# Optimization experiments

Hardware: AMD Instinct MI355X
Metric: run time of the kernel (lower is better)

## Reference

```python
import jax, jax.numpy as jnp
import numpy as np

B = 4; IN_CH = 256; HEAD_CH = 64; NUM_CLS = 3; H = 128; W = 128
NH = 4; KEY = 16; VAL = 16; OUT_CH = 2
VX = 0.1 * 8; VY = 0.1 * 8  # voxel_size[:2] * out_size_factor
DW = 1.6; DL = 3.9; STRIDE = 1
C_CTR = (HEAD_CH + 2 + NUM_CLS) * 9      # 621
C_COR = (HEAD_CH + 2 + NUM_CLS * 4) * 8  # 624
C_FG = (HEAD_CH + 2 + NUM_CLS) * 9       # 621


def _sampler_points():
    offs = np.arange(-STRIDE, STRIDE + 1, STRIDE, dtype=np.float32)
    oy, ox = np.meshgrid(offs, offs, indexing='ij')
    ctr = np.stack([ox, oy], 0).reshape(2, 9)  # pixel offsets
    cx = np.array([-DW/2, -DW/2, DW/2, DW/2, DL/2, -DL/2, DL/2, -DL/2], np.float32) / VX
    cy = np.array([DL/2, -DL/2, DL/2, -DL/2, -DW/2, -DW/2, DW/2, DW/2], np.float32) / VY
    # faithful to torch: stack(dim=1) -> [8,2] then .view(2,8) (row-major reinterpret)
    cor = np.stack([cx, cy], 1).reshape(2, 8)
    r = max(DW, DL)
    fx = np.array([-r/3, -r/3, -r/3, 0, 0, 0, r/3, r/3, r/3], np.float32) / VX
    fy = np.array([-r/3, 0, r/3, -r/3, 0, r/3, -r/3, 0, r/3], np.float32) / VY
    fg = np.stack([fx, fy], 1).reshape(2, 9)
    return jnp.asarray(ctr), jnp.asarray(cor), jnp.asarray(fg)


def _raw_grid():
    gx = jnp.arange(W, dtype=jnp.float32) + 0.5
    gy = jnp.arange(H, dtype=jnp.float32) + 0.5
    return jnp.stack([jnp.broadcast_to(gx[None, :], (H, W)),
                      jnp.broadcast_to(gy[:, None], (H, W))], 0)  # [2,H,W]


def _conv3x3(x, w, b):
    y = jax.lax.conv_general_dilated(x, w, (1, 1), 'SAME',
                                     dimension_numbers=('NCHW', 'OIHW', 'NCHW'))
    return y + b[None, :, None, None]


def _cbr3(x, w, b, s, t):  # conv3x3 + inference-mode BN (folded scale/shift) + relu
    return jax.nn.relu(_conv3x3(x, w, b) * s[None, :, None, None] + t[None, :, None, None])


def _cbr1(x, w, b, s, t):  # per-head 1x1 conv + BN + relu, w: [NH,O,C], x: [B,C,H,W]
    y = jnp.einsum('noc,bchw->nbohw', w, x) + b[:, None, :, None, None]
    return jax.nn.relu(y * s[:, None, :, None, None] + t[:, None, :, None, None])


def _sample(feats, grids):
    # feats [B,C,H,W]; grids [2,n,H,W] pixel coords. Matches F.grid_sample
    # (bilinear, zeros padding, align_corners=False): sample at pixel coord g-0.5.
    n = grids.shape[1]
    geo = jnp.stack([grids[0] / W, grids[1] / H], 0)  # recover_coords, [2,n,H,W]
    gx, gy = grids[0] - 0.5, grids[1] - 0.5
    x0f = jnp.floor(gx); y0f = jnp.floor(gy)
    dx, dy = gx - x0f, gy - y0f
    x0 = x0f.astype(jnp.int32); y0 = y0f.astype(jnp.int32)
    flat = feats.reshape(B, -1, H * W)

    def gather(xc, yc, wgt):
        valid = ((xc >= 0) & (xc < W) & (yc >= 0) & (yc < H)).astype(feats.dtype) * wgt
        idx = jnp.clip(yc, 0, H - 1) * W + jnp.clip(xc, 0, W - 1)
        v = jnp.take(flat, idx.reshape(-1), axis=2).reshape(B, -1, n, H, W)
        return v * valid[None, None]

    s = (gather(x0, y0, (1 - dx) * (1 - dy)) + gather(x0 + 1, y0, dx * (1 - dy))
         + gather(x0, y0 + 1, (1 - dx) * dy) + gather(x0 + 1, y0 + 1, dx * dy))
    geo_b = jnp.broadcast_to(geo[None], (B,) + geo.shape)
    out = jnp.concatenate([s, geo_b], axis=1)  # [B,C+2,n,H,W]
    return out.reshape(B, -1, H, W)           # channel index = c*n + p, as torch .view


def _forward(base_feats, cc_w, cc_b, cc_s, cc_t, ch_w, ch_b,
             oc_w, oc_b, oc_s, oc_t, oh_w, oh_b,
             fc_w, fc_b, fc_s, fc_t, fh_w, fh_b,
             q_w, q_b, q_s, q_t,
             ck_w, ck_b, ck_s, ck_t, cv_w, cv_b, cv_s, cv_t,
             kk_w, kk_b, kk_s, kk_t, kv_w, kv_b, kv_s, kv_t,
             fk_w, fk_b, fk_s, fk_t, fv_w, fv_b, fv_s, fv_t,
             p1_w, p1_b, p1_s, p1_t, p2_w, p2_b):
    center_feat = _cbr3(base_feats, cc_w, cc_b, cc_s, cc_t)
    center_map = _conv3x3(center_feat, ch_w, ch_b)
    corner_feat = _cbr3(base_feats, oc_w, oc_b, oc_s, oc_t)
    corner_map = _conv3x3(corner_feat, oh_w, oh_b)
    fg_feat = _cbr3(base_feats, fc_w, fc_b, fc_s, fc_t)
    fg_map = _conv3x3(fg_feat, fh_w, fh_b)

    ctr_pts, cor_pts, fg_pts = _sampler_points()
    raw = _raw_grid()
    g_ctr = raw[:, None] + ctr_pts[:, :, None, None]  # [2,9,H,W]
    g_cor = raw[:, None] + cor_pts[:, :, None, None]  # [2,8,H,W]
    g_fg = raw[:, None] + fg_pts[:, :, None, None]    # [2,9,H,W]

    cs = _sample(jnp.concatenate([center_feat, center_map], 1), g_ctr)  # [B,621,H,W]
    os_ = _sample(jnp.concatenate([corner_feat, corner_map], 1), g_cor)  # [B,624,H,W]
    fs = _sample(jnp.concatenate([fg_feat, fg_map], 1), g_fg)            # [B,621,H,W]

    q = _cbr1(base_feats, q_w, q_b, q_s, q_t)  # [NH,B,KEY,H,W]
    ck = _cbr1(cs, ck_w, ck_b, ck_s, ck_t); cv = _cbr1(cs, cv_w, cv_b, cv_s, cv_t)
    ok = _cbr1(os_, kk_w, kk_b, kk_s, kk_t); ov = _cbr1(os_, kv_w, kv_b, kv_s, kv_t)
    fk = _cbr1(fs, fk_w, fk_b, fk_s, fk_t); fv = _cbr1(fs, fv_w, fv_b, fv_s, fv_t)

    logits = jnp.stack([(q * ck).sum(2), (q * ok).sum(2), (q * fk).sum(2)], axis=2)  # [NH,B,3,H,W]
    attw = jax.nn.softmax(logits, axis=2)
    vals = jnp.stack([cv, ov, fv], axis=2)          # [NH,B,3,VAL,H,W]
    att = (attw[:, :, :, None] * vals).sum(2)       # [NH,B,VAL,H,W]

    # predict: 1x1 conv over cat([base_feats, att]) + BN + relu, then 1x1 to out_ch
    h1 = (jnp.einsum('noc,bchw->nbohw', p1_w[:, :, :IN_CH], base_feats)
          + jnp.einsum('nov,nbvhw->nbohw', p1_w[:, :, IN_CH:], att)
          + p1_b[:, None, :, None, None])
    h1 = jax.nn.relu(h1 * p1_s[:, None, :, None, None] + p1_t[:, None, :, None, None])
    pred = jnp.einsum('npo,nbohw->nbphw', p2_w, h1) + p2_b[:, None, :, None, None]
    heads = jnp.moveaxis(pred, 0, 1).reshape(B, NH * OUT_CH, H, W)
    return jnp.concatenate([center_map, corner_map, fg_map, heads], axis=1)  # [B,26,H,W]


def setup_inputs() -> dict:
    ks = iter(jax.random.split(jax.random.key(0), 80))

    def rn(shape, s=0.05):
        return jax.random.normal(next(ks), shape, jnp.float32) * s

    d = {"base_feats": jax.random.normal(next(ks), (B, IN_CH, H, W), jnp.float32)}
    for conv, head, hc in (("cc", "ch", NUM_CLS), ("oc", "oh", NUM_CLS * 4), ("fc", "fh", NUM_CLS)):
        d[conv + "_w"] = rn((HEAD_CH, IN_CH, 3, 3)); d[conv + "_b"] = rn((HEAD_CH,))
        d[conv + "_s"] = 1.0 + rn((HEAD_CH,)); d[conv + "_t"] = rn((HEAD_CH,))
        d[head + "_w"] = rn((hc, HEAD_CH, 3, 3)); d[head + "_b"] = jnp.full((hc,), -2.19, jnp.float32)
    d["q_w"] = rn((NH, KEY, IN_CH)); d["q_b"] = rn((NH, KEY))
    d["q_s"] = 1.0 + rn((NH, KEY)); d["q_t"] = rn((NH, KEY))
    for name, cin, cout in (("ck", C_CTR, KEY), ("cv", C_CTR, VAL), ("kk", C_COR, KEY),
                            ("kv", C_COR, VAL), ("fk", C_FG, KEY), ("fv", C_FG, VAL)):
        d[name + "_w"] = rn((NH, cout, cin)); d[name + "_b"] = rn((NH, cout))
        d[name + "_s"] = 1.0 + rn((NH, cout)); d[name + "_t"] = rn((NH, cout))
    d["p1_w"] = rn((NH, HEAD_CH, IN_CH + VAL)); d["p1_b"] = rn((NH, HEAD_CH))
    d["p1_s"] = 1.0 + rn((NH, HEAD_CH)); d["p1_t"] = rn((NH, HEAD_CH))
    d["p2_w"] = rn((NH, OUT_CH, HEAD_CH)); d["p2_b"] = jnp.full((NH, OUT_CH), -2.19, jnp.float32)
    return d


def reference(base_feats, cc_w, cc_b, cc_s, cc_t, ch_w, ch_b,
              oc_w, oc_b, oc_s, oc_t, oh_w, oh_b,
              fc_w, fc_b, fc_s, fc_t, fh_w, fh_b,
              q_w, q_b, q_s, q_t,
              ck_w, ck_b, ck_s, ck_t, cv_w, cv_b, cv_s, cv_t,
              kk_w, kk_b, kk_s, kk_t, kv_w, kv_b, kv_s, kv_t,
              fk_w, fk_b, fk_s, fk_t, fv_w, fv_b, fv_s, fv_t,
              p1_w, p1_b, p1_s, p1_t, p2_w, p2_b):
    return _forward(base_feats, cc_w, cc_b, cc_s, cc_t, ch_w, ch_b,
                    oc_w, oc_b, oc_s, oc_t, oh_w, oh_b,
                    fc_w, fc_b, fc_s, fc_t, fh_w, fh_b,
                    q_w, q_b, q_s, q_t,
                    ck_w, ck_b, ck_s, ck_t, cv_w, cv_b, cv_s, cv_t,
                    kk_w, kk_b, kk_s, kk_t, kv_w, kv_b, kv_s, kv_t,
                    fk_w, fk_b, fk_s, fk_t, fv_w, fv_b, fv_s, fv_t,
                    p1_w, p1_b, p1_s, p1_t, p2_w, p2_b)
```

## Files before the change

### kernel.cpp

```cpp
#include <hip/hip_runtime.h>
#include <hip/hip_bf16.h>
#include <math.h>


#define HW 16384
#define WIMG 128

typedef unsigned short ushortT;
typedef __attribute__((ext_vector_type(8))) short short8;
typedef __attribute__((ext_vector_type(4))) float floatx4;

constexpr size_t OFF_KV    = 16777216;
constexpr size_t OFF_A16   = 29360128;
constexpr size_t OFF_B16   = 38012928;
constexpr size_t OFF_CWT   = 46057216;
constexpr size_t OFF_CB    = OFF_CWT + 442368;
constexpr size_t OFF_HWT   = OFF_CB + 192;
constexpr size_t OFF_QWT   = OFF_HWT + 20736;
constexpr size_t OFF_QB    = OFF_QWT + 16384;
constexpr size_t OFF_KVW   = OFF_QB + 64;
constexpr size_t OFF_GEO   = OFF_KVW + 241664;
constexpr size_t OFF_P1WT  = OFF_GEO + 1152;
constexpr size_t OFF_P1B   = OFF_P1WT + 81920;

struct P53 { const float* p[53]; };

__device__ inline ushortT f2bf(float f) {
    unsigned u = __float_as_uint(f);
    unsigned r = (u + 0x7FFFu + ((u >> 16) & 1u)) >> 16;
    return (ushortT)r;
}
__device__ inline unsigned packbf(float a, float b) {
    return (unsigned)f2bf(a) | ((unsigned)f2bf(b) << 16);
}
__device__ inline float bf2f(ushortT u) {
    return __uint_as_float((unsigned)u << 16);
}

__device__ const float c_ox[3][9] = {
    {-1.f, 0.f, 1.f, -1.f, 0.f, 1.f, -1.f, 0.f, 1.f},
    {-1.f, 2.4375f, -1.f, -2.4375f, 1.f, 2.4375f, 1.f, -2.4375f, 0.f},
    {-1.625f, -1.625f, -1.625f, 0.f, -1.625f, 1.625f, 0.f, -1.625f, 0.f}};
__device__ const float c_oy[3][9] = {
    {-1.f, -1.f, -1.f, 0.f, 0.f, 0.f, 1.f, 1.f, 1.f},
    {2.4375f, -1.f, -2.4375f, -1.f, 2.4375f, 1.f, -2.4375f, 1.f, 0.f},
    {0.f, 0.f, 1.625f, 1.625f, -1.625f, 1.625f, 0.f, 1.625f, 1.625f}};

__device__ const int tapX_cor[16] = {-1,-1, 2, 3,-1,-1,-3,-2, 1, 1, 2, 3, 1, 1,-3,-2};
__device__ const int tapY_cor[16] = { 2, 3,-1,-1,-3,-2,-1,-1, 2, 3, 1, 1,-3,-2, 1, 1};
__device__ const int tapR_cor[16] = { 4, 5, 2, 2, 0, 1, 2, 2, 4, 5, 3, 3, 0, 1, 3, 3};

__device__ inline float cornw(float off, int X) {
    float f = floorf(off);
    float d = off - f;
    int fi = (int)f;
    return (X == fi) ? (1.f - d) : (X == fi + 1) ? d : 0.f;
}

__global__ __launch_bounds__(256) void prep_kernel(P53 ptrs, float* __restrict__ ws) {
    int i = blockIdx.x * 256 + threadIdx.x;
    const float* const* p = ptrs.p;
    if (i < 442368) {
        int tap = i / 49152, r = i % 49152;
        int g = r / 1536, r2 = r % 1536;
        int M = r2 >> 3, j = r2 & 7;
        int br = M >> 6, oc = M & 63, ic = g * 8 + j;
        float v = p[1 + 6 * br][(oc * 256 + ic) * 9 + tap] * p[3 + 6 * br][oc];
        ((ushortT*)(ws + OFF_CWT))[i] = f2bf(v);
        return;
    }
    i -= 442368;
    if (i < 192) {
        int br = i >> 6, oc = i & 63;
        ws[OFF_CB + i] = p[2 + 6 * br][oc] * p[3 + 6 * br][oc] + p[4 + 6 * br][oc];
        return;
    }
    i -= 192;
    if (i < 27648) {
        int j = i & 7, m = (i >> 3) & 15, u = (i >> 7) % 72, br = i / 9216;
        int cnt = (br == 1) ? 12 : 3;
        int t = u >> 3, g = u & 7, ic = g * 8 + j;
        const float* hw = (br == 0) ? p[5] : (br == 1) ? p[11] : p[17];
        float v = (m < cnt) ? hw[(m * 64 + ic) * 9 + t] : 0.f;
        ((ushortT*)(ws + OFF_HWT))[i] = f2bf(v);
        return;
    }
    i -= 27648;
    if (i < 16384) {
        int j = i & 7, m = (i >> 3) & 63, sg = i >> 9;
        int k = (sg >> 2) * 32 + (sg & 3) * 8 + j;
        ((ushortT*)(ws + OFF_QWT))[i] = f2bf(p[19][m * 256 + k] * p[21][m]);
        return;
    }
    i -= 16384;
    if (i < 64) { ws[OFF_QB + i] = p[20][i] * p[21][i] + p[22][i]; return; }
    i -= 64;
    if (i < 483328) {
        int j = i & 7, m = (i >> 3) & 127, ug = i >> 10;
        int br, NG, NT, n, C, chb, ul;
        if (ug < 84)       { br = 0; NG = 9; NT = 9;  n = 9; C = 67; chb = 0;  ul = ug; }
        else if (ug < 164) { br = 1; NG = 5; NT = 16; n = 8; C = 76; chb = 0;  ul = ug - 84; }
        else if (ug < 244) { br = 1; NG = 5; NT = 16; n = 8; C = 76; chb = 40; ul = ug - 164; }
        else               { br = 2; NG = 9; NT = 25; n = 9; C = 67; chb = 0;  ul = ug - 244; }
        int t = ul / NG, g = ul % NG;
        int c = chb + g * 8 + j;
        float v = 0.f;
        if (t < NT && c < C) {
            int X, Y;
            if (br == 0)      { X = t % 3 - 1; Y = t / 3 - 1; }
            else if (br == 1) { X = tapX_cor[t]; Y = tapY_cor[t]; }
            else              { X = t % 5 - 2; Y = t / 5 - 2; }
            const float* wsrc = (m < 64) ? p[23 + 8 * br] : p[27 + 8 * br];
            int mo = (m < 64) ? m : m - 64;
            float sc = (m < 64) ? p[25 + 8 * br][mo] : p[29 + 8 * br][mo];
            int Cn = (C + 2) * n;
            float s = 0.f;
            for (int pp = 0; pp < n; ++pp) {
                float ww = cornw(c_ox[br][pp], X) * cornw(c_oy[br][pp], Y);
                if (ww != 0.f) s += ww * wsrc[mo * Cn + c * n + pp];
            }
            v = s * sc;
        }
        ((ushortT*)(ws + OFF_KVW))[i] = f2bf(v);
        return;
    }
    i -= 483328;
    if (i < 1152) {
        int br = i / 384, rem = i % 384, which = rem >> 7, m = rem & 127;
        int n = (br == 1) ? 8 : 9, C = (br == 1) ? 76 : 67, Cn = (C + 2) * n;
        const float* wsrc = (m < 64) ? p[23 + 8 * br] : p[27 + 8 * br];
        int mo = (m < 64) ? m : m - 64;
        float sc = (m < 64) ? p[25 + 8 * br][mo] : p[29 + 8 * br][mo];
        float bb = (m < 64) ? p[24 + 8 * br][mo] : p[28 + 8 * br][mo];
        float tt = (m < 64) ? p[26 + 8 * br][mo] : p[30 + 8 * br][mo];
        float v = 0.f;
        if (which == 0) {
            for (int pp = 0; pp < n; ++pp) v += wsrc[mo * Cn + C * n + pp];
            v *= sc;
        } else if (which == 1) {
            for (int pp = 0; pp < n; ++pp) v += wsrc[mo * Cn + (C + 1) * n + pp];
            v *= sc;
        } else {
            for (int pp = 0; pp < n; ++pp)
                v += wsrc[mo * Cn + C * n + pp] * c_ox[br][pp]
                   + wsrc[mo * Cn + (C + 1) * n + pp] * c_oy[br][pp];
            v = v * sc * 0.0078125f + bb * sc + tt;
        }
        ws[OFF_GEO + br * 384 + which * 128 + m] = v;
        return;
    }
    i -= 1152;
    if (i < 81920) {
        int j = i & 7, M = (i >> 3) & 255, sg = i >> 11;
        int k = (sg >> 2) * 32 + (sg & 3) * 8 + j;
        int nh = M >> 6, oc = M & 63;
        float sc = p[49][nh * 64 + oc];
        float v;
        if (k < 256) v = p[47][(nh * 64 + oc) * 272 + k] * sc;
        else {
            int k2 = k - 256, nh2 = k2 >> 4, va = k2 & 15;
            v = (nh2 == nh) ? p[47][(nh * 64 + oc) * 272 + 256 + va] * sc : 0.f;
        }
        ((ushortT*)(ws + OFF_P1WT))[i] = f2bf(v);
        return;
    }
    i -= 81920;
    if (i < 256) { ws[OFF_P1B + i] = p[48][i] * p[49][i] + p[50][i]; return; }
}

__global__ __launch_bounds__(256) void pass_a(const float* __restrict__ base,
                                              ushortT* __restrict__ dst) {
    int idx = blockIdx.x * 256 + threadIdx.x;
    if (idx >= 4 * 32 * 130 * 130) return;
    int col = idx % 130, t = idx / 130;
    int row = t % 130; t /= 130;
    int icg = t & 31, b = t >> 5;
    int h = row - 1, w = col - 1;
    unsigned wds[4] = {0u, 0u, 0u, 0u};
    if ((unsigned)h < 128u && (unsigned)w < 128u) {
        const float* s = base + (size_t)(b * 256 + icg * 8) * HW + h * WIMG + w;
        #pragma unroll
        for (int jp = 0; jp < 4; ++jp)
            wds[jp] = packbf(s[(size_t)(2 * jp) * HW], s[(size_t)(2 * jp + 1) * HW]);
    }
    unsigned* d = (unsigned*)(dst + (size_t)idx * 8);
    d[0] = wds[0]; d[1] = wds[1]; d[2] = wds[2]; d[3] = wds[3];
}

__global__ __launch_bounds__(256) void border_zero(ushortT* __restrict__ b16) {
    int idx = blockIdx.x * 256 + threadIdx.x;
    if (idx >= 4 * 28 * 134 * 134) return;
    int col = idx % 134, row = (idx / 134) % 134;
    if (row < 3 || row >= 131 || col < 3 || col >= 131) {
        unsigned* d = (unsigned*)(b16 + (size_t)idx * 8);
        d[0] = 0u; d[1] = 0u; d[2] = 0u; d[3] = 0u;
    }
}

__global__ __launch_bounds__(256) void conv_base_mfma(
    const ushortT* __restrict__ a16, const ushortT* __restrict__ wA,
    const float* __restrict__ cb, ushortT* __restrict__ b16)
{
    const int wv = threadIdx.x >> 6, lane = threadIdx.x & 63;
    const int sub = lane >> 4, ln = lane & 15;
    const int xh = blockIdx.x, h = blockIdx.y, b = blockIdx.z;
    const int x0 = xh * 64;
    __shared__ __align__(16) ushortT sbuf[8 * 3 * 66 * 8];

    floatx4 acc[3][4];
    #pragma unroll
    for (int mt = 0; mt < 3; ++mt)
        #pragma unroll
        for (int nt = 0; nt < 4; ++nt)
            #pragma unroll
            for (int r = 0; r < 4; ++r) acc[mt][nt][r] = 0.f;

    for (int s = 0; s < 4; ++s) {
        __syncthreads();
        for (int it = 0; it < 7; ++it) {
            int idx = threadIdx.x + it * 256;
            if (idx < 1584) {
                int col = idx % 66, t2 = idx / 66;
                int r = t2 % 3, icg = t2 / 3;
                *(short8*)(sbuf + (size_t)idx * 8) = *(const short8*)(a16 +
                    (((size_t)(b * 32 + s * 8 + icg) * 130 + (h + r)) * 130 + (x0 + col)) * 8);
            }
        }
        __syncthreads();
        #pragma unroll
        for (int tap = 0; tap < 9; ++tap) {
            const int ky = tap / 3, kx = tap % 3;
            #pragma unroll
            for (int icc = 0; icc < 2; ++icc) {
                const int icgl = icc * 4 + sub;
                short8 Bf[4];
                #pragma unroll
                for (int nt = 0; nt < 4; ++nt) {
                    int c = nt * 16 + ln + kx;
                    Bf[nt] = *(const short8*)(sbuf + ((icgl * 3 + ky) * 66 + c) * 8);
                }
                const int g = s * 8 + icc * 4 + sub;
                short8 Af[3];
                #pragma unroll
                for (int mt = 0; mt < 3; ++mt) {
                    int m = wv * 48 + mt * 16 + ln;
                    Af[mt] = *(const short8*)(wA + (((size_t)tap * 32 + g) * 192 + m) * 8);
                }
                #pragma unroll
                for (int mt = 0; mt < 3; ++mt)
                    #pragma unroll
                    for (int nt = 0; nt < 4; ++nt)
                        acc[mt][nt] = __builtin_amdgcn_mfma_f32_16x16x32_bf16(
                            Af[mt], Bf[nt], acc[mt][nt], 0, 0, 0);
            }
        }
    }
    #pragma unroll
    for (int mt = 0; mt < 3; ++mt)
        #pragma unroll
        for (int nt = 0; nt < 4; ++nt) {
            int px = x0 + nt * 16 + ln;
            int ocq = wv * 48 + mt * 16 + sub * 4;
            float v0 = fmaxf(acc[mt][nt][0] + cb[ocq + 0], 0.f);
            float v1 = fmaxf(acc[mt][nt][1] + cb[ocq + 1], 0.f);
            float v2 = fmaxf(acc[mt][nt][2] + cb[ocq + 2], 0.f);
            float v3 = fmaxf(acc[mt][nt][3] + cb[ocq + 3], 0.f);
            int br = ocq >> 6, oc = ocq & 63;
            int grp = ((br == 0) ? 0 : (br == 1) ? 9 : 19) + (oc >> 3);
            int j0 = oc & 7;
            unsigned* d = (unsigned*)(b16 +
                (((size_t)(b * 28 + grp) * 134 + (h + 3)) * 134 + (px + 3)) * 8 + j0);
            d[0] = packbf(v0, v1); d[1] = packbf(v2, v3);
        }
}

__global__ __launch_bounds__(256) void conv_head_mfma(
    const ushortT* __restrict__ b16c, const ushortT* __restrict__ wH,
    const float* __restrict__ chb, const float* __restrict__ ohb,
    const float* __restrict__ fhb, float* __restrict__ out,
    ushortT* __restrict__ b16)
{
    const int wv = threadIdx.x >> 6, lane = threadIdx.x & 63;
    const int sub = lane >> 4, ln = lane & 15;
    const int h = blockIdx.x;
    const int br = blockIdx.y % 3, b = blockIdx.y / 3;
    const int cnt = (br == 1) ? 12 : 3;
    const int mapb = (br == 0) ? 0 : (br == 1) ? 3 : 15;
    const int grpb = (br == 0) ? 0 : (br == 1) ? 9 : 19;
    const float* bias = (br == 0) ? chb : (br == 1) ? ohb : fhb;
    __shared__ __align__(16) ushortT sbuf[8 * 3 * 130 * 8];

    for (int it = 0; it < 13; ++it) {
        int idx = threadIdx.x + it * 256;
        if (idx < 3120) {
            int col = idx % 130, t2 = idx / 130;
            int r = t2 % 3, g = t2 / 3;
            *(short8*)(sbuf + (size_t)idx * 8) = *(const short8*)(b16c +
                (((size_t)(b * 28 + grpb + g) * 134 + (h + r + 2)) * 134 + (col + 2)) * 8);
        }
    }
    __syncthreads();

    floatx4 acc[2];
    #pragma unroll
    for (int nt = 0; nt < 2; ++nt)
        #pragma unroll
        for (int r = 0; r < 4; ++r) acc[nt][r] = 0.f;
    #pragma unroll
    for (int k = 0; k < 18; ++k) {
        int u = k * 4 + sub;
        int t = u >> 3, g = u & 7;
        int dxv = t % 3 - 1, ry = t / 3;
        short8 Af = *(const short8*)(wH + ((size_t)(br * 72 + u) * 16 + ln) * 8);
        #pragma unroll
        for (int nt = 0; nt < 2; ++nt) {
            int c = wv * 32 + nt * 16 + ln + dxv + 1;
            short8 Bf = *(const short8*)(sbuf + ((g * 3 + ry) * 130 + c) * 8);
            acc[nt] = __builtin_amdgcn_mfma_f32_16x16x32_bf16(Af, Bf, acc[nt], 0, 0, 0);
        }
    }
    #pragma unroll
    for (int nt = 0; nt < 2; ++nt) {
        int px = wv * 32 + nt * 16 + ln;
        #pragma unroll
        for (int r = 0; r < 4; ++r) {
            int m = sub * 4 + r;
            if (m < cnt) {
                float v = acc[nt][r] + bias[m];
                out[((size_t)b * 26 + mapb + m) * HW + h * WIMG + px] = v;
                int grp = grpb + 8 + (m >> 3), j = m & 7;
                b16[(((size_t)(b * 28 + grp) * 134 + (h + 3)) * 134 + (px + 3)) * 8 + j]
                    = f2bf(v);
            }
        }
    }
}

template<int BR, int NGRP, int NTAP, int ROWS, int COLS, int XMIN, int NCHUNK,
         int NPH, int UBASE>
__global__ __launch_bounds__(256) void kv_conv(
    const ushortT* __restrict__ b16, const ushortT* __restrict__ wU0,
    const float* __restrict__ geo, ushortT* __restrict__ kvout)
{
    const int wv = threadIdx.x >> 6, lane = threadIdx.x & 63;
    const int sub = lane >> 4, ln = lane & 15;
    const int x0 = blockIdx.x * 64, h = blockIdx.y, b = blockIdx.z;
    __shared__ __align__(16) ushortT sbuf[NGRP * ROWS * COLS * 8];

    floatx4 acc[2][4];
    #pragma unroll
    for (int mt = 0; mt < 2; ++mt)
        #pragma unroll
        for (int nt = 0; nt < 4; ++nt)
            #pragma unroll
            for (int r = 0; r < 4; ++r) acc[mt][nt][r] = 0.f;

    #pragma unroll
    for (int ph = 0; ph < NPH; ++ph) {
        const ushortT* wU = wU0 + (size_t)ph * (NCHUNK * 4 * 1024);
        __syncthreads();
        constexpr int NELEM = NGRP * ROWS * COLS;
        for (int it = 0; it < (NELEM + 255) / 256; ++it) {
            int idx = threadIdx.x + it * 256;
            if (idx < NELEM) {
                int col = idx % COLS, t2 = idx / COLS;
                int r = t2 % ROWS, grp = t2 / ROWS;
                int dy = (ROWS == 6) ? ((r < 3) ? r - 3 : r - 2) : (r - ROWS / 2);
                const ushortT* g = b16 +
                    (((size_t)(b * 28 + UBASE + ph * NGRP + grp) * 134 + (h + dy + 3)) * 134
                     + (x0 + col + XMIN + 3)) * 8;
                *(short8*)(sbuf + (size_t)idx * 8) = *(const short8*)g;
            }
        }
        __syncthreads();
        #pragma unroll
        for (int k = 0; k < NCHUNK; ++k) {
            int u = k * 4 + sub;
            int t = u / NGRP, g = u - t * NGRP;
            if (t >= NTAP) t = 0;
            int dxv, ry;
            if (BR == 0)      { dxv = t % 3 - 1; ry = t / 3; }
            else if (BR == 1) { dxv = tapX_cor[t]; ry = tapR_cor[t]; }
            else              { dxv = t % 5 - 2; ry = t / 5; }
            int bbase = (g * ROWS + ry) * COLS + (dxv - XMIN);
            short8 Bf[4];
            #pragma unroll
            for (int nt = 0; nt < 4; ++nt)
                Bf[nt] = *(const short8*)(sbuf + (bbase + nt * 16 + ln) * 8);
            short8 Af[2];
            #pragma unroll
            for (int mt = 0; mt < 2; ++mt)
                Af[mt] = *(const short8*)(wU + ((size_t)u * 128 + wv * 32 + mt * 16 + ln) * 8);
            #pragma unroll
            for (int mt = 0; mt < 2; ++mt)
                #pragma unroll
                for (int nt = 0; nt < 4; ++nt)
                    acc[mt][nt] = __builtin_amdgcn_mfma_f32_16x16x32_bf16(
                        Af[mt], Bf[nt], acc[mt][nt], 0, 0, 0);
        }
    }
    const float fy = (h + 0.5f) * 0.0078125f;
    #pragma unroll
    for (int mt = 0; mt < 2; ++mt)
        #pragma unroll
        for (int nt = 0; nt < 4; ++nt) {
            int px = x0 + nt * 16 + ln;
            float fx = (px + 0.5f) * 0.0078125f;
            #pragma unroll
            for (int r = 0; r < 4; ++r) {
                int Mi = wv * 32 + mt * 16 + sub * 4 + r;
                float v = acc[mt][nt][r] + geo[Mi] * fx + geo[128 + Mi] * fy + geo[256 + Mi];
                kvout[((size_t)(BR * 4 + b) * 128 + Mi) * HW + h * WIMG + px] =
                    f2bf(fmaxf(v, 0.f));
            }
        }
}

__global__ __launch_bounds__(256) void attn_pred_mfma(
    float* __restrict__ ws, const float* __restrict__ p2w,
    const float* __restrict__ p2b, float* __restrict__ out)
{
    const int wv = threadIdx.x >> 6, lane = threadIdx.x & 63;
    const int sub = lane >> 4, ln = lane & 15;
    const int px0 = blockIdx.x * 64, b = blockIdx.y;
    const ushortT* wP1 = (const ushortT*)(ws + OFF_P1WT);
    const ushortT* wQ  = (const ushortT*)(ws + OFF_QWT);
    const ushortT* a16 = (const ushortT*)(ws + OFF_A16);
    const ushortT* kv = (const ushortT*)(ws + OFF_KV);
    const float* p1b = ws + OFF_P1B;
    const float* qb  = ws + OFF_QB;
    __shared__ __align__(16) ushortT xbuf[40 * 64 * 8];
    __shared__ __align__(16) ushortT qld[64 * 64];

    const int mypx = threadIdx.x & 63, nh = threadIdx.x >> 6;
    const int gpx = px0 + mypx, hh = gpx >> 7, ww = gpx & 127;
    #pragma unroll
    for (int g2 = 0; g2 < 8; ++g2) {
        int g = nh * 8 + g2;
        short8 v = *(const short8*)(a16 +
            (((size_t)(b * 32 + g) * 130 + (hh + 1)) * 130 + (ww + 1)) * 8);
        *(short8*)(xbuf + ((size_t)g * 64 + mypx) * 8) = v;
    }
    __syncthreads();

    {
        floatx4 qacc[4];
        #pragma unroll
        for (int nt = 0; nt < 4; ++nt)
            #pragma unroll
            for (int r = 0; r < 4; ++r) qacc[nt][r] = 0.f;
        #pragma unroll
        for (int kk = 0; kk < 8; ++kk) {
            short8 Af = *(const short8*)(wQ + (((kk * 4 + sub) * 64) + wv * 16 + ln) * 8);
            #pragma unroll
            for (int nt = 0; nt < 4; ++nt) {
                short8 Bf = *(const short8*)(xbuf + (((kk * 4 + sub) * 64) + nt * 16 + ln) * 8);
                qacc[nt] = __builtin_amdgcn_mfma_f32_16x16x32_bf16(Af, Bf, qacc[nt], 0, 0, 0);
            }
        }
        #pragma unroll
        for (int nt = 0; nt < 4; ++nt)
            #pragma unroll
            for (int r = 0; r < 4; ++r) {
                int row = wv * 16 + sub * 4 + r;
                qld[row * 64 + nt * 16 + ln] = f2bf(fmaxf(qacc[nt][r] + qb[row], 0.f));
            }
    }
    __syncthreads();

    {
        float l[3];
        #pragma unroll
        for (int br = 0; br < 3; ++br) {
            float s = 0.f;
            #pragma unroll
            for (int ko = 0; ko < 16; ++ko)
                s = fmaf(bf2f(qld[(nh * 16 + ko) * 64 + mypx]),
                         bf2f(kv[(size_t)((br * 4 + b) * 128 + nh * 16 + ko) * HW + gpx]), s);
            l[br] = s;
        }
        float m = fmaxf(l[0], fmaxf(l[1], l[2]));
        float e0 = __expf(l[0] - m), e1 = __expf(l[1] - m), e2 = __expf(l[2] - m);
        float inv = 1.f / (e0 + e1 + e2);
        float aw0 = e0 * inv, aw1 = e1 * inv, aw2 = e2 * inv;
        #pragma unroll
        for (int vap = 0; vap < 8; ++vap) {
            int va0 = vap * 2, va1 = vap * 2 + 1;
            float a0 =
                aw0 * bf2f(kv[(size_t)((0 * 4 + b) * 128 + 64 + nh * 16 + va0) * HW + gpx]) +
                aw1 * bf2f(kv[(size_t)((1 * 4 + b) * 128 + 64 + nh * 16 + va0) * HW + gpx]) +
                aw2 * bf2f(kv[(size_t)((2 * 4 + b) * 128 + 64 + nh * 16 + va0) * HW + gpx]);
            float a1 =
                aw0 * bf2f(kv[(size_t)((0 * 4 + b) * 128 + 64 + nh * 16 + va1) * HW + gpx]) +
                aw1 * bf2f(kv[(size_t)((1 * 4 + b) * 128 + 64 + nh * 16 + va1) * HW + gpx]) +
                aw2 * bf2f(kv[(size_t)((2 * 4 + b) * 128 + 64 + nh * 16 + va1) * HW + gpx]);
            int g = 32 + nh * 2 + (vap >> 2), wo = vap & 3;
            ((unsigned*)xbuf)[(g * 64 + mypx) * 4 + wo] = packbf(a0, a1);
        }
    }
    __syncthreads();

    floatx4 acc[4][4];
    #pragma unroll
    for (int mt = 0; mt < 4; ++mt)
        #pragma unroll
        for (int nt = 0; nt < 4; ++nt)
            #pragma unroll
            for (int r = 0; r < 4; ++r) acc[mt][nt][r] = 0.f;
    #pragma unroll
    for (int kk = 0; kk < 10; ++kk) {
        short8 Bf[4];
        #pragma unroll
        for (int nt = 0; nt < 4; ++nt)
            Bf[nt] = *(const short8*)(xbuf + (((kk * 4 + sub) * 64) + nt * 16 + ln) * 8);
        #pragma unroll
        for (int mt = 0; mt < 4; ++mt) {
            short8 Af = *(const short8*)(wP1 +
                (((size_t)(kk * 4 + sub) * 256) + wv * 64 + mt * 16 + ln) * 8);
            #pragma unroll
            for (int nt = 0; nt < 4; ++nt)
                acc[mt][nt] = __builtin_amdgcn_mfma_f32_16x16x32_bf16(Af, Bf[nt], acc[mt][nt], 0, 0, 0);
        }
    }

    float po0[4] = {0.f, 0.f, 0.f, 0.f}, po1[4] = {0.f, 0.f, 0.f, 0.f};
    #pragma unroll
    for (int mt = 0; mt < 4; ++mt)
        #pragma unroll
        for (int r = 0; r < 4; ++r) {
            int oc = mt * 16 + sub * 4 + r;
            float bias = p1b[wv * 64 + oc];
            float w0 = p2w[(wv * 2 + 0) * 64 + oc];
            float w1 = p2w[(wv * 2 + 1) * 64 + oc];
            #pragma unroll
            for (int nt = 0; nt < 4; ++nt) {
                float hv = fmaxf(acc[mt][nt][r] + bias, 0.f);
                po0[nt] = fmaf(w0, hv, po0[nt]);
                po1[nt] = fmaf(w1, hv, po1[nt]);
            }
        }
    #pragma unroll
    for (int nt = 0; nt < 4; ++nt) {
        po0[nt] += __shfl_xor(po0[nt], 16);
        po0[nt] += __shfl_xor(po0[nt], 32);
        po1[nt] += __shfl_xor(po1[nt], 16);
        po1[nt] += __shfl_xor(po1[nt], 32);
    }
    if (sub == 0) {
        #pragma unroll
        for (int nt = 0; nt < 4; ++nt) {
            int px = px0 + nt * 16 + ln;
            out[((size_t)b * 26 + 18 + wv * 2 + 0) * HW + px] = po0[nt] + p2b[wv * 2 + 0];
            out[((size_t)b * 26 + 18 + wv * 2 + 1) * HW + px] = po1[nt] + p2b[wv * 2 + 1];
        }
    }
}

extern "C" void kernel_launch(void* const* d_in, const int* in_sizes, int n_in,
                              void* d_out, int out_size, void* d_ws, size_t ws_size,
                              hipStream_t stream) {
    (void)in_sizes; (void)n_in; (void)out_size; (void)ws_size;
    float* ws  = (float*)d_ws;
    float* out = (float*)d_out;
    const float* base = (const float*)d_in[0];
    P53 ptrs;
    for (int i = 0; i < 53; ++i) ptrs.p[i] = (const float*)d_in[i];

    ushortT* a16 = (ushortT*)(ws + OFF_A16);
    ushortT* b16 = (ushortT*)(ws + OFF_B16);
    ushortT* kvb = (ushortT*)(ws + OFF_KV);

    prep_kernel<<<4115, 256, 0, stream>>>(ptrs, ws);
    pass_a<<<8450, 256, 0, stream>>>(base, a16);
    border_zero<<<7856, 256, 0, stream>>>(b16);
    conv_base_mfma<<<dim3(2, 128, 4), 256, 0, stream>>>(
        a16, (const ushortT*)(ws + OFF_CWT), ws + OFF_CB, b16);
    conv_head_mfma<<<dim3(128, 12), 256, 0, stream>>>(
        b16, (const ushortT*)(ws + OFF_HWT),
        (const float*)d_in[6], (const float*)d_in[12], (const float*)d_in[18],
        out, b16);

    const ushortT* kvw = (const ushortT*)(ws + OFF_KVW);
    kv_conv<0, 9, 9, 3, 66, -1, 21, 1, 0><<<dim3(2, 128, 4), 256, 0, stream>>>(
        b16, kvw, ws + OFF_GEO, kvb);
    kv_conv<1, 5, 16, 6, 70, -3, 20, 2, 9><<<dim3(2, 128, 4), 256, 0, stream>>>(
        b16, kvw + 86016, ws + OFF_GEO + 384, kvb);
    kv_conv<2, 9, 25, 5, 68, -2, 57, 1, 19><<<dim3(2, 128, 4), 256, 0, stream>>>(
        b16, kvw + 249856, ws + OFF_GEO + 768, kvb);

    attn_pred_mfma<<<dim3(256, 4), 256, 0, stream>>>(ws, (const float*)d_in[51],
                                                     (const float*)d_in[52], out);
}
```

Baseline: 468.6 us.

## Merge KV conv branches into one launch with register double-buffering and prefetch

The three templated kv_conv launches become a single kv_all kernel that picks the branch from blockIdx.z at runtime. Tap offsets move into a shared-memory lookup table, and the warp tiling changes to 2x2 (64 channels by 32 pixels per wave). Fragment loads are double-buffered in registers so they overlap the MFMAs. Separately, pass_a and border_zero are fused into one launch, and conv_base gets a register prefetch of the next input-channel stage. The cost is that runtime branch parameters replace compile-time constants, which may add index math and register pressure.

Result: faster. 446.7 us (-4.7%).

```diff
diff --git a/kernel.cpp b/kernel.cpp
--- a/kernel.cpp
+++ b/kernel.cpp
@@ -168,32 +168,33 @@
     if (i < 256) { ws[OFF_P1B + i] = p[48][i] * p[49][i] + p[50][i]; return; }
 }
 
-__global__ __launch_bounds__(256) void pass_a(const float* __restrict__ base,
-                                              ushortT* __restrict__ dst) {
+__global__ __launch_bounds__(256) void pass_ab(const float* __restrict__ base,
+                                               ushortT* __restrict__ a16,
+                                               ushortT* __restrict__ b16) {
     int idx = blockIdx.x * 256 + threadIdx.x;
-    if (idx >= 4 * 32 * 130 * 130) return;
-    int col = idx % 130, t = idx / 130;
-    int row = t % 130; t /= 130;
-    int icg = t & 31, b = t >> 5;
-    int h = row - 1, w = col - 1;
-    unsigned wds[4] = {0u, 0u, 0u, 0u};
-    if ((unsigned)h < 128u && (unsigned)w < 128u) {
-        const float* s = base + (size_t)(b * 256 + icg * 8) * HW + h * WIMG + w;
-        #pragma unroll
-        for (int jp = 0; jp < 4; ++jp)
-            wds[jp] = packbf(s[(size_t)(2 * jp) * HW], s[(size_t)(2 * jp + 1) * HW]);
-    }
-    unsigned* d = (unsigned*)(dst + (size_t)idx * 8);
-    d[0] = wds[0]; d[1] = wds[1]; d[2] = wds[2]; d[3] = wds[3];
-}
-
-__global__ __launch_bounds__(256) void border_zero(ushortT* __restrict__ b16) {
-    int idx = blockIdx.x * 256 + threadIdx.x;
-    if (idx >= 4 * 28 * 134 * 134) return;
-    int col = idx % 134, row = (idx / 134) % 134;
-    if (row < 3 || row >= 131 || col < 3 || col >= 131) {
-        unsigned* d = (unsigned*)(b16 + (size_t)idx * 8);
-        d[0] = 0u; d[1] = 0u; d[2] = 0u; d[3] = 0u;
+    if (idx < 4 * 32 * 130 * 130) {
+        int col = idx % 130, t = idx / 130;
+        int row = t % 130; t /= 130;
+        int icg = t & 31, b = t >> 5;
+        int h = row - 1, w = col - 1;
+        unsigned wds[4] = {0u, 0u, 0u, 0u};
+        if ((unsigned)h < 128u && (unsigned)w < 128u) {
+            const float* s = base + (size_t)(b * 256 + icg * 8) * HW + h * WIMG + w;
+            #pragma unroll
+            for (int jp = 0; jp < 4; ++jp)
+                wds[jp] = packbf(s[(size_t)(2 * jp) * HW], s[(size_t)(2 * jp + 1) * HW]);
+        }
+        unsigned* d = (unsigned*)(a16 + (size_t)idx * 8);
+        d[0] = wds[0]; d[1] = wds[1]; d[2] = wds[2]; d[3] = wds[3];
+        return;
+    }
+    idx -= 4 * 32 * 130 * 130;
+    if (idx < 4 * 28 * 134 * 134) {
+        int col = idx % 134, row = (idx / 134) % 134;
+        if (row < 3 || row >= 131 || col < 3 || col >= 131) {
+            unsigned* d = (unsigned*)(b16 + (size_t)idx * 8);
+            d[0] = 0u; d[1] = 0u; d[2] = 0u; d[3] = 0u;
+        }
     }
 }
 
@@ -215,18 +216,30 @@
             #pragma unroll
             for (int r = 0; r < 4; ++r) acc[mt][nt][r] = 0.f;
 
-    for (int s = 0; s < 4; ++s) {
-        __syncthreads();
+    short8 pf[7];
+    auto do_loads = [&](int s) {
+        #pragma unroll
         for (int it = 0; it < 7; ++it) {
             int idx = threadIdx.x + it * 256;
             if (idx < 1584) {
                 int col = idx % 66, t2 = idx / 66;
                 int r = t2 % 3, icg = t2 / 3;
-                *(short8*)(sbuf + (size_t)idx * 8) = *(const short8*)(a16 +
+                pf[it] = *(const short8*)(a16 +
                     (((size_t)(b * 32 + s * 8 + icg) * 130 + (h + r)) * 130 + (x0 + col)) * 8);
             }
         }
+    };
+    do_loads(0);
+    #pragma unroll
+    for (int s = 0; s < 4; ++s) {
         __syncthreads();
+        #pragma unroll
+        for (int it = 0; it < 7; ++it) {
+            int idx = threadIdx.x + it * 256;
+            if (idx < 1584) *(short8*)(sbuf + (size_t)idx * 8) = pf[it];
+        }
+        __syncthreads();
+        if (s < 3) do_loads(s + 1);
         #pragma unroll
         for (int tap = 0; tap < 9; ++tap) {
             const int ky = tap / 3, kx = tap % 3;
@@ -336,81 +349,112 @@
     }
 }
 
-template<int BR, int NGRP, int NTAP, int ROWS, int COLS, int XMIN, int NCHUNK,
-         int NPH, int UBASE>
-__global__ __launch_bounds__(256) void kv_conv(
-    const ushortT* __restrict__ b16, const ushortT* __restrict__ wU0,
-    const float* __restrict__ geo, ushortT* __restrict__ kvout)
+__global__ __launch_bounds__(256) void kv_all(
+    const ushortT* __restrict__ b16, const ushortT* __restrict__ kvw,
+    const float* __restrict__ geob, ushortT* __restrict__ kvout)
 {
-    const int wv = threadIdx.x >> 6, lane = threadIdx.x & 63;
+    const int lane = threadIdx.x & 63, wv = threadIdx.x >> 6;
     const int sub = lane >> 4, ln = lane & 15;
-    const int x0 = blockIdx.x * 64, h = blockIdx.y, b = blockIdx.z;
-    __shared__ __align__(16) ushortT sbuf[NGRP * ROWS * COLS * 8];
-
-    floatx4 acc[2][4];
-    #pragma unroll
-    for (int mt = 0; mt < 2; ++mt)
-        #pragma unroll
-        for (int nt = 0; nt < 4; ++nt)
+    const int mw = wv >> 1, nw = wv & 1;
+    const int x0 = blockIdx.x * 64, h = blockIdx.y;
+    const int brv = blockIdx.z >> 2, b = blockIdx.z & 3;
+
+    const int NGRP = (brv == 1) ? 5 : 9;
+    const int NTAP = (brv == 0) ? 9 : (brv == 1) ? 16 : 25;
+    const int ROWS = (brv == 0) ? 3 : (brv == 1) ? 6 : 5;
+    const int COLS = (brv == 0) ? 66 : (brv == 1) ? 70 : 68;
+    const int XMIN = (brv == 0) ? -1 : (brv == 1) ? -3 : -2;
+    const int NCHUNK = (brv == 0) ? 21 : (brv == 1) ? 20 : 57;
+    const int NPH = (brv == 1) ? 2 : 1;
+    const int UBASE = (brv == 0) ? 0 : (brv == 1) ? 9 : 19;
+    const ushortT* wU0 = kvw + ((brv == 0) ? 0 : (brv == 1) ? 86016 : 249856);
+    const float* geo = geob + brv * 384;
+
+    __shared__ __align__(16) ushortT sbuf[3060 * 8];
+    __shared__ int lut[232];
+
+    if (threadIdx.x < 4 * NCHUNK) {
+        int u = threadIdx.x;
+        unsigned Mng = 0xFFFFFFFFu / (unsigned)NGRP + 1u;
+        int t = (int)__umulhi((unsigned)u, Mng);
+        int g = u - t * NGRP;
+        if (t >= NTAP) t = 0;
+        int dxv, ry;
+        if (brv == 0)      { dxv = t % 3 - 1; ry = t / 3; }
+        else if (brv == 1) { dxv = tapX_cor[t]; ry = tapR_cor[t]; }
+        else               { dxv = t % 5 - 2; ry = t / 5; }
+        lut[u] = (g * ROWS + ry) * COLS + (dxv - XMIN);
+    }
+
+    floatx4 acc[4][2];
+    #pragma unroll
+    for (int mt = 0; mt < 4; ++mt)
+        #pragma unroll
+        for (int nt = 0; nt < 2; ++nt)
             #pragma unroll
             for (int r = 0; r < 4; ++r) acc[mt][nt][r] = 0.f;
 
-    #pragma unroll
+    const unsigned Mcols = 0xFFFFFFFFu / (unsigned)COLS + 1u;
+    const unsigned Mrows = 0xFFFFFFFFu / (unsigned)ROWS + 1u;
+    const int NELEM = NGRP * ROWS * COLS;
+
     for (int ph = 0; ph < NPH; ++ph) {
         const ushortT* wU = wU0 + (size_t)ph * (NCHUNK * 4 * 1024);
         __syncthreads();
-        constexpr int NELEM = NGRP * ROWS * COLS;
-        for (int it = 0; it < (NELEM + 255) / 256; ++it) {
-            int idx = threadIdx.x + it * 256;
-            if (idx < NELEM) {
-                int col = idx % COLS, t2 = idx / COLS;
-                int r = t2 % ROWS, grp = t2 / ROWS;
-                int dy = (ROWS == 6) ? ((r < 3) ? r - 3 : r - 2) : (r - ROWS / 2);
-                const ushortT* g = b16 +
-                    (((size_t)(b * 28 + UBASE + ph * NGRP + grp) * 134 + (h + dy + 3)) * 134
-                     + (x0 + col + XMIN + 3)) * 8;
-                *(short8*)(sbuf + (size_t)idx * 8) = *(const short8*)g;
-            }
+        for (int idx = threadIdx.x; idx < NELEM; idx += 256) {
+            int row = (int)__umulhi((unsigned)idx, Mcols);
+            int col = idx - row * COLS;
+            int grp = (int)__umulhi((unsigned)row, Mrows);
+            int rw = row - grp * ROWS;
+            int dy = (ROWS == 6) ? ((rw < 3) ? rw - 3 : rw - 2) : (rw - (ROWS >> 1));
+            *(short8*)(sbuf + (size_t)idx * 8) = *(const short8*)(b16 +
+                (((size_t)(b * 28 + UBASE + ph * NGRP + grp) * 134 + (h + dy + 3)) * 134
+                 + (x0 + col + XMIN + 3)) * 8);
         }
         __syncthreads();
-        #pragma unroll
-        for (int k = 0; k < NCHUNK; ++k) {
+
+        short8 A0[4], B0[2], A1[4], B1[2];
+        auto ldf = [&](int k, short8 A[4], short8 B[2]) {
             int u = k * 4 + sub;
-            int t = u / NGRP, g = u - t * NGRP;
-            if (t >= NTAP) t = 0;
-            int dxv, ry;
-            if (BR == 0)      { dxv = t % 3 - 1; ry = t / 3; }
-            else if (BR == 1) { dxv = tapX_cor[t]; ry = tapR_cor[t]; }
-            else              { dxv = t % 5 - 2; ry = t / 5; }
-            int bbase = (g * ROWS + ry) * COLS + (dxv - XMIN);
-            short8 Bf[4];
-            #pragma unroll
-            for (int nt = 0; nt < 4; ++nt)
-                Bf[nt] = *(const short8*)(sbuf + (bbase + nt * 16 + ln) * 8);
-            short8 Af[2];
-            #pragma unroll
-            for (int mt = 0; mt < 2; ++mt)
-                Af[mt] = *(const short8*)(wU + ((size_t)u * 128 + wv * 32 + mt * 16 + ln) * 8);
-            #pragma unroll
-            for (int mt = 0; mt < 2; ++mt)
+            int bb = lut[u];
+            const ushortT* wp = wU + (size_t)u * 1024;
+            #pragma unroll
+            for (int mt = 0; mt < 4; ++mt)
+                A[mt] = *(const short8*)(wp + (mw * 64 + mt * 16 + ln) * 8);
+            #pragma unroll
+            for (int nt = 0; nt < 2; ++nt)
+                B[nt] = *(const short8*)(sbuf + (size_t)(bb + nw * 32 + nt * 16 + ln) * 8);
+        };
+        auto dom = [&](short8 A[4], short8 B[2]) {
+            #pragma unroll
+            for (int mt = 0; mt < 4; ++mt)
                 #pragma unroll
-                for (int nt = 0; nt < 4; ++nt)
+                for (int nt = 0; nt < 2; ++nt)
                     acc[mt][nt] = __builtin_amdgcn_mfma_f32_16x16x32_bf16(
-                        Af[mt], Bf[nt], acc[mt][nt], 0, 0, 0);
-        }
-    }
+                        A[mt], B[nt], acc[mt][nt], 0, 0, 0);
+        };
+        ldf(0, A0, B0);
+        for (int k = 0; k < NCHUNK; k += 2) {
+            bool h1 = (k + 1 < NCHUNK);
+            if (h1) ldf(k + 1, A1, B1);
+            dom(A0, B0);
+            if (k + 2 < NCHUNK) ldf(k + 2, A0, B0);
+            if (h1) dom(A1, B1);
+        }
+    }
+
     const float fy = (h + 0.5f) * 0.0078125f;
     #pragma unroll
-    for (int mt = 0; mt < 2; ++mt)
-        #pragma unroll
-        for (int nt = 0; nt < 4; ++nt) {
-            int px = x0 + nt * 16 + ln;
+    for (int mt = 0; mt < 4; ++mt)
+        #pragma unroll
+        for (int nt = 0; nt < 2; ++nt) {
+            int px = x0 + nw * 32 + nt * 16 + ln;
             float fx = (px + 0.5f) * 0.0078125f;
             #pragma unroll
             for (int r = 0; r < 4; ++r) {
-                int Mi = wv * 32 + mt * 16 + sub * 4 + r;
+                int Mi = mw * 64 + mt * 16 + sub * 4 + r;
                 float v = acc[mt][nt][r] + geo[Mi] * fx + geo[128 + Mi] * fy + geo[256 + Mi];
-                kvout[((size_t)(BR * 4 + b) * 128 + Mi) * HW + h * WIMG + px] =
+                kvout[((size_t)(brv * 4 + b) * 128 + Mi) * HW + h * WIMG + px] =
                     f2bf(fmaxf(v, 0.f));
             }
         }
@@ -571,23 +615,15 @@
     ushortT* kvb = (ushortT*)(ws + OFF_KV);
 
     prep_kernel<<<4115, 256, 0, stream>>>(ptrs, ws);
-    pass_a<<<8450, 256, 0, stream>>>(base, a16);
-    border_zero<<<7856, 256, 0, stream>>>(b16);
+    pass_ab<<<16306, 256, 0, stream>>>(base, a16, b16);
     conv_base_mfma<<<dim3(2, 128, 4), 256, 0, stream>>>(
         a16, (const ushortT*)(ws + OFF_CWT), ws + OFF_CB, b16);
     conv_head_mfma<<<dim3(128, 12), 256, 0, stream>>>(
         b16, (const ushortT*)(ws + OFF_HWT),
         (const float*)d_in[6], (const float*)d_in[12], (const float*)d_in[18],
         out, b16);
-
-    const ushortT* kvw = (const ushortT*)(ws + OFF_KVW);
-    kv_conv<0, 9, 9, 3, 66, -1, 21, 1, 0><<<dim3(2, 128, 4), 256, 0, stream>>>(
-        b16, kvw, ws + OFF_GEO, kvb);
-    kv_conv<1, 5, 16, 6, 70, -3, 20, 2, 9><<<dim3(2, 128, 4), 256, 0, stream>>>(
-        b16, kvw + 86016, ws + OFF_GEO + 384, kvb);
-    kv_conv<2, 9, 25, 5, 68, -2, 57, 1, 19><<<dim3(2, 128, 4), 256, 0, stream>>>(
-        b16, kvw + 249856, ws + OFF_GEO + 768, kvb);
-
+    kv_all<<<dim3(2, 128, 12), 256, 0, stream>>>(
+        b16, (const ushortT*)(ws + OFF_KVW), ws + OFF_GEO, kvb);
     attn_pred_mfma<<<dim3(256, 4), 256, 0, stream>>>(ws, (const float*)d_in[51],
                                                      (const float*)d_in[52], out);
 }
```
